# Kernel tuning notes

Hardware: AMD Instinct MI355X
Metric: run time of the kernel (lower is better)

Reference implementation:

```python
import jax, jax.numpy as jnp
import numpy as np

D_MODEL = 1024
D_HIDDEN = 32   # per-head MPS bond dimension
N_HEADS = 8
D_FF = 4096
EPS_LN = 1e-5
EPS_NORM = 1e-6


def layernorm(x, g, b):
    m = jnp.mean(x, axis=-1, keepdims=True)
    v = jnp.mean(jnp.square(x - m), axis=-1, keepdims=True)
    return (x - m) * jax.lax.rsqrt(v + EPS_LN) * g + b


def mps_recurrence(x, Wa, ba, h0, Wo, bo):
    # x: [B,S,D]. Per-token per-head transfer matrices A_t in R^{dh x dh}.
    B, S, D = x.shape
    A = (x @ Wa + ba).reshape(B, S, N_HEADS, D_HIDDEN, D_HIDDEN)
    A = jnp.moveaxis(A, 1, 0)  # [S,B,H,dh,dh]
    h_init = jnp.broadcast_to(h0, (B, N_HEADS, D_HIDDEN))  # [B,H,dh]

    def step(h, A_t):
        h = jnp.einsum('bhij,bhj->bhi', A_t, h)
        h = h / (jnp.linalg.norm(h, axis=-1, keepdims=True) + EPS_NORM)
        return h, h

    _, ys = jax.lax.scan(step, h_init, A)          # ys: [S,B,H,dh]
    ys = jnp.moveaxis(ys, 0, 1).reshape(B, S, N_HEADS * D_HIDDEN)
    return ys @ Wo + bo                            # [B,S,D]


def setup_inputs() -> dict:
    key = jax.random.key(0)
    ks = jax.random.split(key, 12)
    B, S, D = 4, 2048, D_MODEL
    inv = 1.0 / np.sqrt(D)
    inv_hd = 1.0 / np.sqrt(N_HEADS * D_HIDDEN)
    return {
        'x': jax.random.normal(ks[0], (B, S, D), jnp.float32),
        'ln1_g': jnp.ones((D,), jnp.float32),
        'ln1_b': jnp.zeros((D,), jnp.float32),
        'Wa': jax.random.normal(ks[1], (D, N_HEADS * D_HIDDEN * D_HIDDEN), jnp.float32) * inv,
        'ba': jnp.zeros((N_HEADS * D_HIDDEN * D_HIDDEN,), jnp.float32),
        'h0': jax.random.normal(ks[2], (N_HEADS, D_HIDDEN), jnp.float32) / np.sqrt(D_HIDDEN),
        'Wo': jax.random.normal(ks[3], (N_HEADS * D_HIDDEN, D), jnp.float32) * inv_hd,
        'bo': jnp.zeros((D,), jnp.float32),
        'ln2_g': jnp.ones((D,), jnp.float32),
        'ln2_b': jnp.zeros((D,), jnp.float32),
        'W1': jax.random.normal(ks[4], (D, D_FF), jnp.float32) * inv,
        'b1': jnp.zeros((D_FF,), jnp.float32),
        'W2': jax.random.normal(ks[5], (D_FF, D), jnp.float32) / np.sqrt(D_FF),
        'b2': jnp.zeros((D,), jnp.float32),
    }


def reference(x, ln1_g, ln1_b, Wa, ba, h0, Wo, bo, ln2_g, ln2_b, W1, b1, W2, b2):
    # Dropout in eval mode (identity).
    x = x + mps_recurrence(layernorm(x, ln1_g, ln1_b), Wa, ba, h0, Wo, bo)
    h = layernorm(x, ln2_g, ln2_b)
    ffn = jax.nn.gelu(h @ W1 + b1, approximate=False) @ W2 + b2
    return x + ffn
```

## Files before the change

### kernel.cpp

```cpp
#include <hip/hip_runtime.h>
#include <hip/hip_bf16.h>
#include <math.h>

typedef float f32x4 __attribute__((ext_vector_type(4)));
typedef __bf16 bf16x4 __attribute__((ext_vector_type(4)));
typedef __bf16 bf16x8 __attribute__((ext_vector_type(8)));

#define AS1(p) ((const __attribute__((address_space(1))) void*)(p))
#define AS3(p) ((__attribute__((address_space(3))) void*)(p))

static constexpr int D_MODEL = 1024;
static constexpr int S_LEN   = 2048;
static constexpr int BATCH   = 4;
static constexpr int NTOK    = BATCH * S_LEN;
static constexpr int NH      = 8;
static constexpr int DH      = 32;
static constexpr int NA      = NH * DH * DH;
static constexpr int D_FF    = 4096;
static constexpr int CHUNK   = 16;
static constexpr int NCHUNK  = S_LEN / CHUNK;

__device__ __forceinline__ void xcd_swizzle(int& bx, int& by) {
  int gx = gridDim.x;
  int orig = by * gx + bx;
  int r8 = orig & 7, j = orig >> 3;
  int bxn = j % gx, grp = j / gx;
  bx = bxn;
  by = grp * 8 + r8;
}

__device__ __forceinline__ float gelu_erf_fast(float v) {
  float z = fabsf(v) * 0.70710678118654752f;
  float t = __builtin_amdgcn_rcpf(fmaf(0.3275911f, z, 1.0f));
  float p = t * (0.254829592f + t * (-0.284496736f + t * (1.421413741f +
            t * (-1.453152027f + t * 1.061405429f))));
  float e = __builtin_amdgcn_exp2f(-1.4426950408889634f * z * z);
  float er = 1.0f - p * e;
  er = (v < 0.0f) ? -er : er;
  return 0.5f * v * (1.0f + er);
}

__global__ __launch_bounds__(256) void transpose_bf16(
    const float* __restrict__ in, __bf16* __restrict__ out, int R, int C) {
  __shared__ float tile[32][33];
  int tx = threadIdx.x & 31, ty = threadIdx.x >> 5;
  int c0 = blockIdx.x * 32, r0 = blockIdx.y * 32;
  for (int i = ty; i < 32; i += 8)
    tile[i][tx] = in[(size_t)(r0 + i) * C + c0 + tx];
  __syncthreads();
  for (int i = ty; i < 32; i += 8)
    out[(size_t)(c0 + i) * R + r0 + tx] = (__bf16)tile[tx][i];
}

__global__ __launch_bounds__(256) void transpose_split(
    const float* __restrict__ in, __bf16* __restrict__ ohi,
    __bf16* __restrict__ olo, int R, int C) {
  __shared__ float tile[32][33];
  int tx = threadIdx.x & 31, ty = threadIdx.x >> 5;
  int c0 = blockIdx.x * 32, r0 = blockIdx.y * 32;
  for (int i = ty; i < 32; i += 8)
    tile[i][tx] = in[(size_t)(r0 + i) * C + c0 + tx];
  __syncthreads();
  for (int i = ty; i < 32; i += 8) {
    float v = tile[tx][i];
    __bf16 h = (__bf16)v;
    ohi[(size_t)(c0 + i) * R + r0 + tx] = h;
    olo[(size_t)(c0 + i) * R + r0 + tx] = (__bf16)(v - (float)h);
  }
}

template <int MODE>
__global__ __launch_bounds__(256) void ln_kernel(
    const float* __restrict__ in, const float* __restrict__ g,
    const float* __restrict__ bta, void* __restrict__ outv,
    void* __restrict__ outv2) {
  int row = blockIdx.x, tid = threadIdx.x;
  const float4* in4 = (const float4*)(in + (size_t)row * D_MODEL);
  float4 v = in4[tid];
  float s  = v.x + v.y + v.z + v.w;
  float ss = v.x * v.x + v.y * v.y + v.z * v.z + v.w * v.w;
  for (int o = 32; o; o >>= 1) { s += __shfl_down(s, o); ss += __shfl_down(ss, o); }
  __shared__ float ps[4], pq[4];
  int lane = tid & 63, w = tid >> 6;
  if (lane == 0) { ps[w] = s; pq[w] = ss; }
  __syncthreads();
  s  = ps[0] + ps[1] + ps[2] + ps[3];
  ss = pq[0] + pq[1] + pq[2] + pq[3];
  float mean = s * (1.0f / D_MODEL);
  float var  = ss * (1.0f / D_MODEL) - mean * mean;
  float inv  = rsqrtf(fmaxf(var, 0.0f) + 1e-5f);
  float4 gv = ((const float4*)g)[tid];
  float4 bv = ((const float4*)bta)[tid];
  float o0 = (v.x - mean) * inv * gv.x + bv.x;
  float o1 = (v.y - mean) * inv * gv.y + bv.y;
  float o2 = (v.z - mean) * inv * gv.z + bv.z;
  float o3 = (v.w - mean) * inv * gv.w + bv.w;
  if (MODE == 1) {
    float4 o = {o0, o1, o2, o3};
    ((float4*)outv)[(size_t)row * (D_MODEL / 4) + tid] = o;
  } else if (MODE == 0) {
    bf16x4 o;
    o[0] = (__bf16)o0; o[1] = (__bf16)o1; o[2] = (__bf16)o2; o[3] = (__bf16)o3;
    ((bf16x4*)outv)[(size_t)row * (D_MODEL / 4) + tid] = o;
  } else {
    bf16x4 oh, ol;
    oh[0] = (__bf16)o0; oh[1] = (__bf16)o1; oh[2] = (__bf16)o2; oh[3] = (__bf16)o3;
    ol[0] = (__bf16)(o0 - (float)oh[0]);
    ol[1] = (__bf16)(o1 - (float)oh[1]);
    ol[2] = (__bf16)(o2 - (float)oh[2]);
    ol[3] = (__bf16)(o3 - (float)oh[3]);
    ((bf16x4*)outv )[(size_t)row * (D_MODEL / 4) + tid] = oh;
    ((bf16x4*)outv2)[(size_t)row * (D_MODEL / 4) + tid] = ol;
  }
}

enum { EPI_BF16_BIAS = 0, EPI_BF16_BIAS_GELU = 1, EPI_F32_BIAS_RES = 2,
       EPI_F32_BIAS_ONLY = 3 };

#define SB0() __builtin_amdgcn_sched_barrier(0)
#define BARRIER()                                      \
  do {                                                 \
    SB0();                                             \
    __builtin_amdgcn_s_barrier();                      \
    SB0();                                             \
  } while (0)
#define LGKM0()                                        \
  do {                                                 \
    asm volatile("s_waitcnt lgkmcnt(0)" ::: "memory"); \
    SB0();                                             \
  } while (0)
#define GEMM8_QUAD(I0, J0)                                                   \
  do {                                                                       \
    __builtin_amdgcn_s_setprio(1);                                           \
    _Pragma("unroll") for (int i_ = 0; i_ < 4; ++i_)                         \
    _Pragma("unroll") for (int j_ = 0; j_ < 2; ++j_)                         \
    _Pragma("unroll") for (int k_ = 0; k_ < 2; ++k_)                         \
      acc[(I0) + i_][(J0) + j_] = __builtin_amdgcn_mfma_f32_16x16x32_bf16(   \
          a[(I0) + i_][k_], b[(J0) + j_][k_], acc[(I0) + i_][(J0) + j_],     \
          0, 0, 0);                                                          \
    __builtin_amdgcn_s_setprio(0);                                           \
  } while (0)

template <int SPLIT, int EPI>
__global__ __launch_bounds__(512, 2) void gemm8(
    const __bf16* __restrict__ pA, const __bf16* __restrict__ pA2,
    const __bf16* __restrict__ pB, const __bf16* __restrict__ pB2,
    const float* __restrict__ bias, void* __restrict__ out,
    int M, int N, int K) {
  __shared__ alignas(16) char lds[131072];
  const int tid = threadIdx.x;
  const int lane = tid & 63, w = tid >> 6;
  const int fm = lane & 15, fq = lane >> 4;
  const int wm2 = w >> 2, wn4 = w & 3;
  int bx = blockIdx.x, by = blockIdx.y;
  xcd_swizzle(bx, by);
  const int m0 = by * 256, n0 = bx * 256;
  const int NT = SPLIT ? 48 : (K >> 6);
  const int KS = SPLIT ? D_MODEL : K;

  const int lrow8 = lane >> 3;
  const int lslot = ((lane & 7) ^ lrow8) << 3;

  auto stageA = [&](int kt, int h) {
    const __bf16* base = SPLIT ? ((kt < 32) ? pA : pA2) : pA;
    int kc = SPLIT ? ((kt & 15) << 6) : (kt << 6);
    char* d0 = lds + ((kt & 1) << 15);
#pragma unroll
    for (int j = 0; j < 2; ++j) {
      int rb = h * 128 + j * 64 + w * 8;
      const __bf16* src = base + (size_t)(m0 + rb + lrow8) * KS + kc + lslot;
      __builtin_amdgcn_global_load_lds(AS1(src), AS3(d0 + rb * 128 + lane * 16), 16, 0, 0);
    }
  };
  auto stageB = [&](int kt, int h) {
    const __bf16* base = SPLIT ? ((kt >= 16 && kt < 32) ? pB2 : pB) : pB;
    int kc = SPLIT ? ((kt & 15) << 6) : (kt << 6);
    char* d0 = lds + 65536 + ((kt & 1) << 15);
#pragma unroll
    for (int j = 0; j < 2; ++j) {
      int rb = h * 128 + j * 64 + w * 8;
      const __bf16* src = base + (size_t)(n0 + rb + lrow8) * KS + kc + lslot;
      __builtin_amdgcn_global_load_lds(AS1(src), AS3(d0 + rb * 128 + lane * 16), 16, 0, 0);
    }
  };
  auto rdA = [&](int bo, int i, int ks) -> bf16x8 {
    int row = wm2 * 128 + i * 16 + fm;
    return *(const bf16x8*)(lds + bo + row * 128 +
                            ((((ks << 2) + fq) ^ (row & 7)) << 4));
  };
  auto rdB = [&](int bo, int j, int ks) -> bf16x8 {
    int row = wn4 * 64 + j * 16 + fm;
    return *(const bf16x8*)(lds + 65536 + bo + row * 128 +
                            ((((ks << 2) + fq) ^ (row & 7)) << 4));
  };

  f32x4 acc[8][4];
#pragma unroll
  for (int i = 0; i < 8; ++i)
#pragma unroll
    for (int j = 0; j < 4; ++j)
#pragma unroll
      for (int r = 0; r < 4; ++r) acc[i][j][r] = 0.0f;

  stageA(0, 0); stageA(0, 1); stageB(0, 0); stageB(0, 1);
  if (NT > 1) stageA(1, 0);
  SB0();
  if (NT > 1) asm volatile("s_waitcnt vmcnt(2)" ::: "memory");
  else        asm volatile("s_waitcnt vmcnt(0)" ::: "memory");
  BARRIER();
  bf16x8 a[8][2], b[4][2];
#pragma unroll
  for (int i = 0; i < 4; ++i) { a[i][0] = rdA(0, i, 0); a[i][1] = rdA(0, i, 1); }
#pragma unroll
  for (int j = 0; j < 2; ++j) { b[j][0] = rdB(0, j, 0); b[j][1] = rdB(0, j, 1); }

  for (int t = 0; t < NT; ++t) {
    const int bo  = (t & 1) << 15;
    const int bon = ((t + 1) & 1) << 15;
    BARRIER();
    if (t + 1 < NT) { stageA(t + 1, 1); stageB(t + 1, 0); }
    LGKM0();
#pragma unroll
    for (int j = 2; j < 4; ++j) { b[j][0] = rdB(bo, j, 0); b[j][1] = rdB(bo, j, 1); }
    SB0();
    GEMM8_QUAD(0, 0);
    BARRIER();
    if (t + 1 < NT) stageB(t + 1, 1);
    LGKM0();
#pragma unroll
    for (int i = 4; i < 8; ++i) { a[i][0] = rdA(bo, i, 0); a[i][1] = rdA(bo, i, 1); }
    SB0();
    GEMM8_QUAD(0, 2);
    BARRIER();
    LGKM0();
    GEMM8_QUAD(4, 0);
    BARRIER();
    if (t + 2 < NT) stageA(t + 2, 0);
    SB0();
    if (t + 1 < NT) {
      if (t + 2 < NT) asm volatile("s_waitcnt vmcnt(2)" ::: "memory");
      else            asm volatile("s_waitcnt vmcnt(0)" ::: "memory");
      BARRIER();
#pragma unroll
      for (int i = 0; i < 4; ++i) { a[i][0] = rdA(bon, i, 0); a[i][1] = rdA(bon, i, 1); }
#pragma unroll
      for (int j = 0; j < 2; ++j) { b[j][0] = rdB(bon, j, 0); b[j][1] = rdB(bon, j, 1); }
      SB0();
    }
    GEMM8_QUAD(4, 2);
  }
  __syncthreads();

  if (EPI == EPI_F32_BIAS_ONLY) {
    float* outF = (float*)out;
#pragma unroll
    for (int j = 0; j < 4; ++j) {
      int col = n0 + wn4 * 64 + j * 16 + fm;
      float bv = bias[col];
#pragma unroll
      for (int i = 0; i < 8; ++i)
#pragma unroll
        for (int r = 0; r < 4; ++r) {
          int row = m0 + wm2 * 128 + i * 16 + fq * 4 + r;
          outF[(size_t)row * N + col] = acc[i][j][r] + bv;
        }
    }
  } else {
    char* patch = lds + w * 16384;
    float bv4[4];
#pragma unroll
    for (int j = 0; j < 4; ++j) bv4[j] = bias[n0 + wn4 * 64 + j * 16 + fm];
#pragma unroll
    for (int i = 0; i < 8; ++i)
#pragma unroll
      for (int j = 0; j < 4; ++j)
#pragma unroll
        for (int r = 0; r < 4; ++r) {
          float v = gelu_erf_fast(acc[i][j][r] + bv4[j]);
          *(__bf16*)(patch + (i * 16 + fq * 4 + r) * 128 + (j * 16 + fm) * 2) =
              (__bf16)v;
        }
    asm volatile("s_waitcnt lgkmcnt(0)" ::: "memory");
#pragma unroll
    for (int rr = 0; rr < 16; ++rr) {
      bf16x8 ov = *(const bf16x8*)(patch + (rr * 8 + lrow8) * 128 + (lane & 7) * 16);
      size_t grow = (size_t)(m0 + wm2 * 128 + rr * 8 + lrow8);
      *(bf16x8*)((__bf16*)out + grow * N + n0 + wn4 * 64 + (lane & 7) * 8) = ov;
    }
  }
}

template <int EPI>
__global__ __launch_bounds__(256) void gemm_bf16(
    const __bf16* __restrict__ Amat, const __bf16* __restrict__ BT,
    const float* __restrict__ bias, const float* __restrict__ res,
    void* __restrict__ out, int M, int N, int K) {
  __shared__ __bf16 smem[2 * 128 * 32];
  __bf16* As = smem;
  __bf16* Bs = smem + 128 * 32;
  const int tid = threadIdx.x;
  const int lane = tid & 63, w = tid >> 6;
  int bx = blockIdx.x, by = blockIdx.y;
  xcd_swizzle(bx, by);
  const int m0 = by * 128, n0 = bx * 128;
  const int wm = (w >> 1) * 64, wn = (w & 1) * 64;

  f32x4 acc[4][4];
#pragma unroll
  for (int a = 0; a < 4; a++)
#pragma unroll
    for (int b = 0; b < 4; b++)
#pragma unroll
      for (int r = 0; r < 4; r++) acc[a][b][r] = 0.0f;

  const int srow = tid >> 2;
  const int soff = (tid & 3) * 16;
  const __bf16* gA0 = Amat + (size_t)(m0 + srow) * K + (soff >> 1);
  const __bf16* gA1 = Amat + (size_t)(m0 + srow + 64) * K + (soff >> 1);
  const __bf16* gB0 = BT + (size_t)(n0 + srow) * K + (soff >> 1);
  const __bf16* gB1 = BT + (size_t)(n0 + srow + 64) * K + (soff >> 1);
  char* lA0 = (char*)As + srow * 64 + soff;
  char* lA1 = (char*)As + (srow + 64) * 64 + soff;
  char* lB0 = (char*)Bs + srow * 64 + soff;
  char* lB1 = (char*)Bs + (srow + 64) * 64 + soff;

  const int fm = lane & 15, fq = lane >> 4;
  for (int k0 = 0; k0 < K; k0 += 32) {
    __builtin_amdgcn_global_load_lds(AS1(gA0 + k0), AS3(lA0), 16, 0, 0);
    __builtin_amdgcn_global_load_lds(AS1(gA1 + k0), AS3(lA1), 16, 0, 0);
    __builtin_amdgcn_global_load_lds(AS1(gB0 + k0), AS3(lB0), 16, 0, 0);
    __builtin_amdgcn_global_load_lds(AS1(gB1 + k0), AS3(lB1), 16, 0, 0);
    __syncthreads();
    bf16x8 af[4], bf[4];
#pragma unroll
    for (int t = 0; t < 4; t++)
      af[t] = *(const bf16x8*)((const char*)As + (wm + t * 16 + fm) * 64 + fq * 16);
#pragma unroll
    for (int t = 0; t < 4; t++)
      bf[t] = *(const bf16x8*)((const char*)Bs + (wn + t * 16 + fm) * 64 + fq * 16);
#pragma unroll
    for (int tm = 0; tm < 4; tm++)
#pragma unroll
      for (int tn = 0; tn < 4; tn++)
        acc[tm][tn] = __builtin_amdgcn_mfma_f32_16x16x32_bf16(af[tm], bf[tn], acc[tm][tn], 0, 0, 0);
    __syncthreads();
  }

#pragma unroll
  for (int tn = 0; tn < 4; tn++) {
    int col = n0 + wn + tn * 16 + fm;
    float bv = bias[col];
#pragma unroll
    for (int tm = 0; tm < 4; tm++) {
#pragma unroll
      for (int r = 0; r < 4; r++) {
        int row = m0 + wm + tm * 16 + fq * 4 + r;
        float v = acc[tm][tn][r] + bv;
        size_t idx = (size_t)row * N + col;
        if (EPI == EPI_F32_BIAS_RES) {
          ((float*)out)[idx] = v + res[idx];
        } else if (EPI == EPI_BF16_BIAS_GELU) {
          v = gelu_erf_fast(v);
          ((__bf16*)out)[idx] = (__bf16)v;
        } else {
          ((__bf16*)out)[idx] = (__bf16)v;
        }
      }
    }
  }
}

__global__ __launch_bounds__(64) void mps_chunkprod_f32(
    float* __restrict__ A) {
  int bid = blockIdx.x;
  int c = bid & 127, hh = bid >> 7;
  int lane = threadIdx.x;
  int jj = lane & 31, half = lane >> 5;
  __shared__ float Albuf[2][DH * DH];

  float curc[32];
#pragma unroll
  for (int k = 0; k < 32; k++) curc[k] = (k == jj) ? 1.0f : 0.0f;

  float* Abase = A + (size_t)(c * CHUNK) * NA + (size_t)hh * (DH * DH);

  {
    const float4* src = (const float4*)Abase;
    float4* dst = (float4*)Albuf[0];
#pragma unroll
    for (int r = 0; r < 4; r++) dst[lane + 64 * r] = src[lane + 64 * r];
  }
  __syncthreads();

  for (int t = 0; t < CHUNK; t++) {
    int cb = t & 1;
    float4 pf[4];
    if (t + 1 < CHUNK) {
      const float4* srcn = (const float4*)(Abase + (size_t)(t + 1) * NA);
#pragma unroll
      for (int r = 0; r < 4; r++) pf[r] = srcn[lane + 64 * r];
    }
    float nxt[16];
#pragma unroll
    for (int i16 = 0; i16 < 16; i16++) {
      const float4* ap = (const float4*)&Albuf[cb][(half * 16 + i16) * 32];
      float a0 = 0.f, a1 = 0.f, a2 = 0.f, a3 = 0.f;
#pragma unroll
      for (int k4 = 0; k4 < 8; k4++) {
        float4 av = ap[k4];
        a0 += av.x * curc[k4 * 4 + 0];
        a1 += av.y * curc[k4 * 4 + 1];
        a2 += av.z * curc[k4 * 4 + 2];
        a3 += av.w * curc[k4 * 4 + 3];
      }
      nxt[i16] = (a0 + a1) + (a2 + a3);
    }
    {
      float* slot = Abase + (size_t)t * NA;
#pragma unroll
      for (int i16 = 0; i16 < 16; i16++)
        slot[(half * 16 + i16) * 32 + jj] = nxt[i16];
    }
#pragma unroll
    for (int i16 = 0; i16 < 16; i16++) {
      float mine  = nxt[i16];
      float other = __shfl_xor(mine, 32);
      curc[i16]      = (half == 0) ? mine  : other;
      curc[16 + i16] = (half == 0) ? other : mine;
    }
    if (t + 1 < CHUNK) {
      float4* dst = (float4*)Albuf[cb ^ 1];
#pragma unroll
      for (int r = 0; r < 4; r++) dst[lane + 64 * r] = pf[r];
      __syncthreads();
    }
  }
}

__global__ __launch_bounds__(64) void mps_chunkscan(
    const float* __restrict__ pref, const float* __restrict__ h0,
    float* __restrict__ hstart) {
  int hh = blockIdx.x;
  int lane = threadIdx.x, i = lane & 31, half = lane >> 5;
  float hv = h0[hh * 32 + i];
  const size_t cstride = (size_t)CHUNK * NA;
  const float* row = pref + (size_t)(CHUNK - 1) * NA + (size_t)hh * (DH * DH)
                     + i * 32 + half * 16;
  int kb = half * 16;

  float4 pf0[4], pf1[4];
#pragma unroll
  for (int r = 0; r < 4; r++) pf0[r] = ((const float4*)row)[r];
#pragma unroll
  for (int r = 0; r < 4; r++) pf1[r] = ((const float4*)(row + cstride))[r];

  for (int c = 0; c < NCHUNK; c++) {
    if (lane < 32) hstart[((size_t)hh * NCHUNK + c) * 32 + i] = hv;
    float4 cur[4];
#pragma unroll
    for (int r = 0; r < 4; r++) cur[r] = pf0[r];
#pragma unroll
    for (int r = 0; r < 4; r++) pf0[r] = pf1[r];
    int cn = (c + 2 < NCHUNK) ? (c + 2) : (NCHUNK - 1);
#pragma unroll
    for (int r = 0; r < 4; r++)
      pf1[r] = ((const float4*)(row + (size_t)cn * cstride))[r];

    float a0 = 0.f, a1 = 0.f, a2 = 0.f, a3 = 0.f;
#pragma unroll
    for (int j4 = 0; j4 < 4; j4++) {
      float4 pv = cur[j4];
      a0 += pv.x * __shfl(hv, kb + j4 * 4 + 0);
      a1 += pv.y * __shfl(hv, kb + j4 * 4 + 1);
      a2 += pv.z * __shfl(hv, kb + j4 * 4 + 2);
      a3 += pv.w * __shfl(hv, kb + j4 * 4 + 3);
    }
    float y = (a0 + a1) + (a2 + a3);
    y += __shfl_xor(y, 32);
    float nn = y * y;
#pragma unroll
    for (int o = 16; o; o >>= 1) nn += __shfl_xor(nn, o);
    hv = y / (sqrtf(nn) + 1e-6f);
  }
}

__global__ __launch_bounds__(256) void mps_expand_par(
    const float* __restrict__ pref, const float* __restrict__ hstart,
    __bf16* __restrict__ ys, int tok0base) {
  int w = threadIdx.x >> 6, lane = threadIdx.x & 63;
  int i = lane & 31, half = lane >> 5;
  int task = blockIdx.x * 4 + w;
  int hh = task & 7, tok = task >> 3;
  int c = tok >> 4;
  int kb = half * 16;

  float hv = hstart[((size_t)hh * NCHUNK + c) * 32 + i];
  const float4* Mr = (const float4*)(pref + (size_t)tok * NA
                     + (size_t)hh * (DH * DH) + i * 32 + half * 16);
  float4 m0 = Mr[0], m1 = Mr[1], m2 = Mr[2], m3 = Mr[3];

  float a0 = 0.f, a1 = 0.f, a2 = 0.f, a3 = 0.f;
  a0 += m0.x * __shfl(hv, kb + 0);  a1 += m0.y * __shfl(hv, kb + 1);
  a2 += m0.z * __shfl(hv, kb + 2);  a3 += m0.w * __shfl(hv, kb + 3);
  a0 += m1.x * __shfl(hv, kb + 4);  a1 += m1.y * __shfl(hv, kb + 5);
  a2 += m1.z * __shfl(hv, kb + 6);  a3 += m1.w * __shfl(hv, kb + 7);
  a0 += m2.x * __shfl(hv, kb + 8);  a1 += m2.y * __shfl(hv, kb + 9);
  a2 += m2.z * __shfl(hv, kb + 10); a3 += m2.w * __shfl(hv, kb + 11);
  a0 += m3.x * __shfl(hv, kb + 12); a1 += m3.y * __shfl(hv, kb + 13);
  a2 += m3.z * __shfl(hv, kb + 14); a3 += m3.w * __shfl(hv, kb + 15);
  float y = (a0 + a1) + (a2 + a3);
  y += __shfl_xor(y, 32);
  float nn = y * y;
#pragma unroll
  for (int o = 16; o; o >>= 1) nn += __shfl_xor(nn, o);
  float hvo = y / (sqrtf(nn) + 1e-6f);
  if (lane < 32)
    ys[(size_t)(tok0base + tok) * (NH * DH) + hh * 32 + i] = (__bf16)hvo;
}

extern "C" void kernel_launch(void* const* d_in, const int* in_sizes, int n_in,
                              void* d_out, int out_size, void* d_ws, size_t ws_size,
                              hipStream_t stream) {
  const float* x     = (const float*)d_in[0];
  const float* ln1_g = (const float*)d_in[1];
  const float* ln1_b = (const float*)d_in[2];
  const float* Wa    = (const float*)d_in[3];
  const float* ba    = (const float*)d_in[4];
  const float* h0    = (const float*)d_in[5];
  const float* Wo    = (const float*)d_in[6];
  const float* bo    = (const float*)d_in[7];
  const float* ln2_g = (const float*)d_in[8];
  const float* ln2_b = (const float*)d_in[9];
  const float* W1    = (const float*)d_in[10];
  const float* b1    = (const float*)d_in[11];
  const float* W2    = (const float*)d_in[12];
  const float* b2    = (const float*)d_in[13];
  float* out = (float*)d_out;

  char* wsb = (char*)d_ws;
  size_t off = 0;
  auto alloc = [&](size_t bytes) -> void* {
    void* p = wsb + off;
    off += (bytes + 255) & ~(size_t)255;
    return p;
  };
  __bf16* WoT   = (__bf16*)alloc((size_t)(NH * DH) * D_MODEL * 2);
  __bf16* W1T   = (__bf16*)alloc((size_t)D_MODEL * D_FF * 2);
  __bf16* W2T   = (__bf16*)alloc((size_t)D_FF * D_MODEL * 2);
  __bf16* ys    = (__bf16*)alloc((size_t)NTOK * NH * DH * 2);
  float*  hst   = (float*) alloc((size_t)NH * NCHUNK * DH * 4);
  __bf16* xnh   = (__bf16*)alloc((size_t)NTOK * D_MODEL * 2);
  __bf16* xnl   = (__bf16*)alloc((size_t)NTOK * D_MODEL * 2);
  __bf16* WaTh  = (__bf16*)alloc((size_t)D_MODEL * NA * 2);
  __bf16* WaTl  = (__bf16*)alloc((size_t)D_MODEL * NA * 2);
  size_t tail0 = off;
  float*  Af32 = (float*) alloc((size_t)S_LEN * NA * 4);
  __bf16* mid  = (__bf16*)(wsb + tail0);

  transpose_bf16<<<dim3(D_MODEL / 32, (NH * DH) / 32), 256, 0, stream>>>(Wo, WoT, NH * DH, D_MODEL);
  transpose_bf16<<<dim3(D_FF / 32, D_MODEL / 32), 256, 0, stream>>>(W1, W1T, D_MODEL, D_FF);
  transpose_bf16<<<dim3(D_MODEL / 32, D_FF / 32), 256, 0, stream>>>(W2, W2T, D_FF, D_MODEL);
  transpose_split<<<dim3(NA / 32, D_MODEL / 32), 256, 0, stream>>>(Wa, WaTh, WaTl, D_MODEL, NA);

  ln_kernel<2><<<NTOK, 256, 0, stream>>>(x, ln1_g, ln1_b, xnh, xnl);

  for (int b = 0; b < BATCH; b++) {
    gemm8<1, EPI_F32_BIAS_ONLY><<<dim3(NA / 256, S_LEN / 256), 512, 0, stream>>>(
        xnh + (size_t)b * S_LEN * D_MODEL, xnl + (size_t)b * S_LEN * D_MODEL,
        WaTh, WaTl, ba, Af32, S_LEN, NA, D_MODEL);
    mps_chunkprod_f32<<<NH * NCHUNK, 64, 0, stream>>>(Af32);
    mps_chunkscan<<<NH, 64, 0, stream>>>(Af32, h0, hst);
    mps_expand_par<<<(S_LEN * NH) / 4, 256, 0, stream>>>(Af32, hst, ys, b * S_LEN);
  }

  gemm_bf16<EPI_F32_BIAS_RES><<<dim3(D_MODEL / 128, NTOK / 128), 256, 0, stream>>>(
      ys, WoT, bo, x, out, NTOK, D_MODEL, NH * DH);

  ln_kernel<0><<<NTOK, 256, 0, stream>>>(out, ln2_g, ln2_b, xnh, nullptr);

  gemm8<0, EPI_BF16_BIAS_GELU><<<dim3(D_FF / 256, NTOK / 256), 512, 0, stream>>>(
      xnh, nullptr, W1T, nullptr, b1, mid, NTOK, D_FF, D_MODEL);

  gemm_bf16<EPI_F32_BIAS_RES><<<dim3(D_MODEL / 128, NTOK / 128), 256, 0, stream>>>(
      mid, W2T, b2, out, out, NTOK, D_MODEL, D_FF);
}
```

Before: 1.452 ms.

## Fuse split-bf16 Wa GEMM into single-pass kernel and narrow N tiles for Wo/W2 GEMMs

Replaces the 48-k-step split-precision Wa GEMM with a dedicated kernel. It stages the hi/lo parts of both operands for each k-tile once and computes the hi*hi, hi*lo and lo*hi products from the same LDS tiles, with interleaved prefetch and explicit vmcnt waits. This cuts repeated global loads and loop overhead, but the kernel now uses the full 128KB of LDS and runs one block per CU. The Wo and W2 GEMMs switch to 128x64 tiles, which doubles their grid to fill more CUs at the cost of lower per-block reuse.

```diff
diff --git a/kernel.cpp b/kernel.cpp
--- a/kernel.cpp
+++ b/kernel.cpp
@@ -129,17 +129,148 @@
     asm volatile("s_waitcnt lgkmcnt(0)" ::: "memory"); \
     SB0();                                             \
   } while (0)
-#define GEMM8_QUAD(I0, J0)                                                   \
+#define VMCNT(n)                                                  \
+  do {                                                            \
+    SB0();                                                        \
+    asm volatile("s_waitcnt vmcnt(" #n ")" ::: "memory");         \
+    SB0();                                                        \
+  } while (0)
+#define QUADN(A_, B_, I0, J0)                                                \
   do {                                                                       \
     __builtin_amdgcn_s_setprio(1);                                           \
     _Pragma("unroll") for (int i_ = 0; i_ < 4; ++i_)                         \
     _Pragma("unroll") for (int j_ = 0; j_ < 2; ++j_)                         \
     _Pragma("unroll") for (int k_ = 0; k_ < 2; ++k_)                         \
       acc[(I0) + i_][(J0) + j_] = __builtin_amdgcn_mfma_f32_16x16x32_bf16(   \
-          a[(I0) + i_][k_], b[(J0) + j_][k_], acc[(I0) + i_][(J0) + j_],     \
+          A_[(I0) + i_][k_], B_[(J0) + j_][k_], acc[(I0) + i_][(J0) + j_],   \
           0, 0, 0);                                                          \
     __builtin_amdgcn_s_setprio(0);                                           \
   } while (0)
+
+__global__ __launch_bounds__(512, 1) void gemm8_split3(
+    const __bf16* __restrict__ Ah, const __bf16* __restrict__ Al,
+    const __bf16* __restrict__ Bh, const __bf16* __restrict__ Bl,
+    const float* __restrict__ bias, float* __restrict__ out,
+    int M, int N, int K) {
+  __shared__ alignas(16) char lds[131072];
+  const int SAH = 0, SAL = 32768, SBH = 65536, SBL = 98304;
+  const int tid = threadIdx.x, lane = tid & 63, w = tid >> 6;
+  const int fm = lane & 15, fq = lane >> 4;
+  const int wm2 = w >> 2, wn4 = w & 3;
+  int bx = blockIdx.x, by = blockIdx.y;
+  xcd_swizzle(bx, by);
+  const int m0 = by * 256, n0 = bx * 256;
+  const int NT = K >> 6;
+  const int lrow8 = lane >> 3;
+  const int lslot = ((lane & 7) ^ lrow8) << 3;
+
+  auto stage = [&](const __bf16* base, int r0g, int kc, int slot) {
+#pragma unroll
+    for (int jj = 0; jj < 4; ++jj) {
+      int rb = jj * 64 + w * 8;
+      const __bf16* src = base + (size_t)(r0g + rb + lrow8) * K + kc + lslot;
+      __builtin_amdgcn_global_load_lds(AS1(src),
+          AS3(lds + slot + rb * 128 + lane * 16), 16, 0, 0);
+    }
+  };
+  auto rdM = [&](int slot, int i, int ks) -> bf16x8 {
+    int row = wm2 * 128 + i * 16 + fm;
+    return *(const bf16x8*)(lds + slot + row * 128 +
+                            ((((ks << 2) + fq) ^ (row & 7)) << 4));
+  };
+  auto rdN = [&](int slot, int j, int ks) -> bf16x8 {
+    int row = wn4 * 64 + j * 16 + fm;
+    return *(const bf16x8*)(lds + slot + row * 128 +
+                            ((((ks << 2) + fq) ^ (row & 7)) << 4));
+  };
+
+  f32x4 acc[8][4];
+#pragma unroll
+  for (int i = 0; i < 8; ++i)
+#pragma unroll
+    for (int j = 0; j < 4; ++j)
+#pragma unroll
+      for (int r = 0; r < 4; ++r) acc[i][j][r] = 0.0f;
+
+  stage(Ah, m0, 0, SAH); stage(Al, m0, 0, SAL);
+  stage(Bh, n0, 0, SBH); stage(Bl, n0, 0, SBL);
+  VMCNT(0);
+  BARRIER();
+  bf16x8 aH[8][2], aL[8][2], bH[4][2], bL[4][2];
+#pragma unroll
+  for (int i = 0; i < 4; ++i) { aH[i][0] = rdM(SAH, i, 0); aH[i][1] = rdM(SAH, i, 1); }
+#pragma unroll
+  for (int j = 0; j < 4; ++j) { bH[j][0] = rdN(SBH, j, 0); bH[j][1] = rdN(SBH, j, 1); }
+
+  for (int s = 0; s < NT; ++s) {
+    const bool more = (s + 1 < NT);
+    const int kc1 = (s + 1) << 6;
+    BARRIER();
+    if (more) stage(Bh, n0, kc1, SBH);
+    SB0();
+#pragma unroll
+    for (int i = 4; i < 8; ++i) { aH[i][0] = rdM(SAH, i, 0); aH[i][1] = rdM(SAH, i, 1); }
+    SB0();
+    QUADN(aH, bH, 0, 0); QUADN(aH, bH, 0, 2);
+    if (more) VMCNT(8); else VMCNT(4);
+    BARRIER();
+    if (more) stage(Ah, m0, kc1, SAH);
+    SB0();
+#pragma unroll
+    for (int j = 0; j < 4; ++j) { bL[j][0] = rdN(SBL, j, 0); bL[j][1] = rdN(SBL, j, 1); }
+    SB0();
+    QUADN(aH, bH, 4, 0); QUADN(aH, bH, 4, 2);
+    BARRIER();
+    if (more) stage(Bl, n0, kc1, SBL);
+    SB0();
+    QUADN(aH, bL, 0, 0); QUADN(aH, bL, 0, 2);
+    if (more) VMCNT(12); else VMCNT(0);
+    BARRIER();
+#pragma unroll
+    for (int i = 0; i < 4; ++i) { aL[i][0] = rdM(SAL, i, 0); aL[i][1] = rdM(SAL, i, 1); }
+    SB0();
+    QUADN(aH, bL, 4, 0); QUADN(aH, bL, 4, 2);
+    BARRIER();
+#pragma unroll
+    for (int i = 4; i < 8; ++i) { aL[i][0] = rdM(SAL, i, 0); aL[i][1] = rdM(SAL, i, 1); }
+    SB0();
+    QUADN(aL, bH, 0, 0); QUADN(aL, bH, 0, 2);
+    BARRIER();
+    if (more) {
+      stage(Al, m0, kc1, SAL);
+      VMCNT(8);
+    }
+    BARRIER();
+    if (more) {
+#pragma unroll
+      for (int i = 0; i < 4; ++i) { aH[i][0] = rdM(SAH, i, 0); aH[i][1] = rdM(SAH, i, 1); }
+      SB0();
+    }
+    QUADN(aL, bH, 4, 0); QUADN(aL, bH, 4, 2);
+    if (more) {
+      SB0();
+#pragma unroll
+      for (int j = 0; j < 4; ++j) { bH[j][0] = rdN(SBH, j, 0); bH[j][1] = rdN(SBH, j, 1); }
+      SB0();
+    }
+  }
+
+  float* outF = (float*)out;
+#pragma unroll
+  for (int j = 0; j < 4; ++j) {
+    int col = n0 + wn4 * 64 + j * 16 + fm;
+    float bv = bias[col];
+#pragma unroll
+    for (int i = 0; i < 8; ++i)
+#pragma unroll
+      for (int r = 0; r < 4; ++r) {
+        int row = m0 + wm2 * 128 + i * 16 + fq * 4 + r;
+        outF[(size_t)row * N + col] = acc[i][j][r] + bv;
+      }
+  }
+}
+
+#define GEMM8_QUAD(I0, J0) QUADN(a, b, I0, J0)
 
 template <int SPLIT, int EPI>
 __global__ __launch_bounds__(512, 2) void gemm8(
@@ -155,31 +286,29 @@
   int bx = blockIdx.x, by = blockIdx.y;
   xcd_swizzle(bx, by);
   const int m0 = by * 256, n0 = bx * 256;
-  const int NT = SPLIT ? 48 : (K >> 6);
-  const int KS = SPLIT ? D_MODEL : K;
+  const int NT = K >> 6;
+  const int KS = K;
 
   const int lrow8 = lane >> 3;
   const int lslot = ((lane & 7) ^ lrow8) << 3;
 
   auto stageA = [&](int kt, int h) {
-    const __bf16* base = SPLIT ? ((kt < 32) ? pA : pA2) : pA;
-    int kc = SPLIT ? ((kt & 15) << 6) : (kt << 6);
+    int kc = kt << 6;
     char* d0 = lds + ((kt & 1) << 15);
 #pragma unroll
     for (int j = 0; j < 2; ++j) {
       int rb = h * 128 + j * 64 + w * 8;
-      const __bf16* src = base + (size_t)(m0 + rb + lrow8) * KS + kc + lslot;
+      const __bf16* src = pA + (size_t)(m0 + rb + lrow8) * KS + kc + lslot;
       __builtin_amdgcn_global_load_lds(AS1(src), AS3(d0 + rb * 128 + lane * 16), 16, 0, 0);
     }
   };
   auto stageB = [&](int kt, int h) {
-    const __bf16* base = SPLIT ? ((kt >= 16 && kt < 32) ? pB2 : pB) : pB;
-    int kc = SPLIT ? ((kt & 15) << 6) : (kt << 6);
+    int kc = kt << 6;
     char* d0 = lds + 65536 + ((kt & 1) << 15);
 #pragma unroll
     for (int j = 0; j < 2; ++j) {
       int rb = h * 128 + j * 64 + w * 8;
-      const __bf16* src = base + (size_t)(n0 + rb + lrow8) * KS + kc + lslot;
+      const __bf16* src = pB + (size_t)(n0 + rb + lrow8) * KS + kc + lslot;
       __builtin_amdgcn_global_load_lds(AS1(src), AS3(d0 + rb * 128 + lane * 16), 16, 0, 0);
     }
   };
@@ -291,25 +420,24 @@
 }
 
 template <int EPI>
-__global__ __launch_bounds__(256) void gemm_bf16(
+__global__ __launch_bounds__(256) void gemm_n64(
     const __bf16* __restrict__ Amat, const __bf16* __restrict__ BT,
     const float* __restrict__ bias, const float* __restrict__ res,
     void* __restrict__ out, int M, int N, int K) {
-  __shared__ __bf16 smem[2 * 128 * 32];
-  __bf16* As = smem;
-  __bf16* Bs = smem + 128 * 32;
+  __shared__ __bf16 As[128 * 32];
+  __shared__ __bf16 Bs[64 * 32];
   const int tid = threadIdx.x;
   const int lane = tid & 63, w = tid >> 6;
   int bx = blockIdx.x, by = blockIdx.y;
   xcd_swizzle(bx, by);
-  const int m0 = by * 128, n0 = bx * 128;
-  const int wm = (w >> 1) * 64, wn = (w & 1) * 64;
-
-  f32x4 acc[4][4];
+  const int m0 = by * 128, n0 = bx * 64;
+  const int wm = (w >> 1) * 64, wn = (w & 1) * 32;
+
+  f32x4 acc[4][2];
 #pragma unroll
   for (int a = 0; a < 4; a++)
 #pragma unroll
-    for (int b = 0; b < 4; b++)
+    for (int b = 0; b < 2; b++)
 #pragma unroll
       for (int r = 0; r < 4; r++) acc[a][b][r] = 0.0f;
 
@@ -318,36 +446,33 @@
   const __bf16* gA0 = Amat + (size_t)(m0 + srow) * K + (soff >> 1);
   const __bf16* gA1 = Amat + (size_t)(m0 + srow + 64) * K + (soff >> 1);
   const __bf16* gB0 = BT + (size_t)(n0 + srow) * K + (soff >> 1);
-  const __bf16* gB1 = BT + (size_t)(n0 + srow + 64) * K + (soff >> 1);
   char* lA0 = (char*)As + srow * 64 + soff;
   char* lA1 = (char*)As + (srow + 64) * 64 + soff;
   char* lB0 = (char*)Bs + srow * 64 + soff;
-  char* lB1 = (char*)Bs + (srow + 64) * 64 + soff;
 
   const int fm = lane & 15, fq = lane >> 4;
   for (int k0 = 0; k0 < K; k0 += 32) {
     __builtin_amdgcn_global_load_lds(AS1(gA0 + k0), AS3(lA0), 16, 0, 0);
     __builtin_amdgcn_global_load_lds(AS1(gA1 + k0), AS3(lA1), 16, 0, 0);
     __builtin_amdgcn_global_load_lds(AS1(gB0 + k0), AS3(lB0), 16, 0, 0);
-    __builtin_amdgcn_global_load_lds(AS1(gB1 + k0), AS3(lB1), 16, 0, 0);
     __syncthreads();
-    bf16x8 af[4], bf[4];
+    bf16x8 af[4], bf[2];
 #pragma unroll
     for (int t = 0; t < 4; t++)
       af[t] = *(const bf16x8*)((const char*)As + (wm + t * 16 + fm) * 64 + fq * 16);
 #pragma unroll
-    for (int t = 0; t < 4; t++)
+    for (int t = 0; t < 2; t++)
       bf[t] = *(const bf16x8*)((const char*)Bs + (wn + t * 16 + fm) * 64 + fq * 16);
 #pragma unroll
     for (int tm = 0; tm < 4; tm++)
 #pragma unroll
-      for (int tn = 0; tn < 4; tn++)
+      for (int tn = 0; tn < 2; tn++)
         acc[tm][tn] = __builtin_amdgcn_mfma_f32_16x16x32_bf16(af[tm], bf[tn], acc[tm][tn], 0, 0, 0);
     __syncthreads();
   }
 
 #pragma unroll
-  for (int tn = 0; tn < 4; tn++) {
+  for (int tn = 0; tn < 2; tn++) {
     int col = n0 + wn + tn * 16 + fm;
     float bv = bias[col];
 #pragma unroll
@@ -359,9 +484,6 @@
         size_t idx = (size_t)row * N + col;
         if (EPI == EPI_F32_BIAS_RES) {
           ((float*)out)[idx] = v + res[idx];
-        } else if (EPI == EPI_BF16_BIAS_GELU) {
-          v = gelu_erf_fast(v);
-          ((__bf16*)out)[idx] = (__bf16)v;
         } else {
           ((__bf16*)out)[idx] = (__bf16)v;
         }
@@ -565,7 +687,7 @@
   ln_kernel<2><<<NTOK, 256, 0, stream>>>(x, ln1_g, ln1_b, xnh, xnl);
 
   for (int b = 0; b < BATCH; b++) {
-    gemm8<1, EPI_F32_BIAS_ONLY><<<dim3(NA / 256, S_LEN / 256), 512, 0, stream>>>(
+    gemm8_split3<<<dim3(NA / 256, S_LEN / 256), 512, 0, stream>>>(
         xnh + (size_t)b * S_LEN * D_MODEL, xnl + (size_t)b * S_LEN * D_MODEL,
         WaTh, WaTl, ba, Af32, S_LEN, NA, D_MODEL);
     mps_chunkprod_f32<<<NH * NCHUNK, 64, 0, stream>>>(Af32);
@@ -573,7 +695,7 @@
     mps_expand_par<<<(S_LEN * NH) / 4, 256, 0, stream>>>(Af32, hst, ys, b * S_LEN);
   }
 
-  gemm_bf16<EPI_F32_BIAS_RES><<<dim3(D_MODEL / 128, NTOK / 128), 256, 0, stream>>>(
+  gemm_n64<EPI_F32_BIAS_RES><<<dim3(D_MODEL / 64, NTOK / 128), 256, 0, stream>>>(
       ys, WoT, bo, x, out, NTOK, D_MODEL, NH * DH);
 
   ln_kernel<0><<<NTOK, 256, 0, stream>>>(out, ln2_g, ln2_b, xnh, nullptr);
@@ -581,6 +703,6 @@
   gemm8<0, EPI_BF16_BIAS_GELU><<<dim3(D_FF / 256, NTOK / 256), 512, 0, stream>>>(
       xnh, nullptr, W1T, nullptr, b1, mid, NTOK, D_FF, D_MODEL);
 
-  gemm_bf16<EPI_F32_BIAS_RES><<<dim3(D_MODEL / 128, NTOK / 128), 256, 0, stream>>>(
+  gemm_n64<EPI_F32_BIAS_RES><<<dim3(D_MODEL / 64, NTOK / 128), 256, 0, stream>>>(
       mid, W2T, b2, out, out, NTOK, D_MODEL, D_FF);
 }
```

Measured after the change: 2.459 ms. 69.4% more time.
